# Kernel tuning notes

Hardware: AMD Instinct MI355X
Metric: run time of the kernel (lower is better)

## Reference

```python
import jax, jax.numpy as jnp
import numpy as np

D = 512
N_TISSUES = 200
N_MECH = 6
WINDOW = 32
LN_EPS = 1e-5


def _make_params(key):
    ks = jax.random.split(key, 16)
    p = {}
    def lin(k, fin, fout):
        return jax.random.normal(k, (fin, fout), jnp.float32) * 0.02, jnp.zeros((fout,), jnp.float32)
    for s in ('local', 'regional', 'macro'):
        p[f'ln_g_{s}'] = jnp.ones((D,), jnp.float32)
        p[f'ln_b_{s}'] = jnp.zeros((D,), jnp.float32)
    p['W_fuse'], p['b_fuse'] = lin(ks[0], 3 * D, D)
    p['W_i1'], p['b_i1'] = lin(ks[1], D, D // 2)
    p['W_i2'], p['b_i2'] = lin(ks[2], D // 2, 1)
    p['W_t1'], p['b_t1'] = lin(ks[3], D, D)
    p['W_t2'], p['b_t2'] = lin(ks[4], D, N_TISSUES)
    p['W_m1'], p['b_m1'] = lin(ks[5], D, D // 2)
    p['W_m2'], p['b_m2'] = lin(ks[6], D // 2, N_MECH)
    return p


def setup_inputs() -> dict:
    key = jax.random.key(0)
    ks = jax.random.split(key, 8)
    B, L = 16, 4096
    inp = {}
    names = ['ref_local', 'ref_regional', 'ref_macro', 'alt_local', 'alt_regional', 'alt_macro']
    for i, n in enumerate(names):
        inp[n] = jax.random.normal(ks[i], (B, L, D), jnp.float32)
    inp['variant_pos'] = jax.random.randint(ks[6], (B,), 0, L, jnp.int32)
    inp.update(_make_params(ks[7]))
    return inp


def _diff_pool(ref, alt, pos, gamma, beta):
    # Vectorized version of the per-batch boundary-clamped window gather:
    # window [pos-w, pos+w] intersected with [0, L), diff = alt-ref, mean-pool.
    B, L, Dm = ref.shape
    offs = jnp.arange(-WINDOW, WINDOW + 1)          # (2w+1,)
    idx = pos[:, None] + offs[None, :]               # (B, 2w+1)
    valid = (idx >= 0) & (idx < L)                   # boundary clamp mask
    idxc = jnp.clip(idx, 0, L - 1)
    r = jnp.take_along_axis(ref, idxc[:, :, None], axis=1)   # (B, 2w+1, D)
    a = jnp.take_along_axis(alt, idxc[:, :, None], axis=1)
    diff = (a - r) * valid[:, :, None].astype(ref.dtype)
    pooled = diff.sum(axis=1) / valid.sum(axis=1)[:, None].astype(ref.dtype)  # (B, D)
    mu = pooled.mean(axis=-1, keepdims=True)
    var = ((pooled - mu) ** 2).mean(axis=-1, keepdims=True)
    return (pooled - mu) / jnp.sqrt(var + LN_EPS) * gamma + beta


def _gelu(x):
    return jax.nn.gelu(x, approximate=False)


def reference(ref_local, ref_regional, ref_macro, alt_local, alt_regional, alt_macro,
              variant_pos,
              ln_g_local, ln_b_local, ln_g_regional, ln_b_regional, ln_g_macro, ln_b_macro,
              W_fuse, b_fuse, W_i1, b_i1, W_i2, b_i2,
              W_t1, b_t1, W_t2, b_t2, W_m1, b_m1, W_m2, b_m2):
    d_local = _diff_pool(ref_local, alt_local, variant_pos, ln_g_local, ln_b_local)
    d_reg = _diff_pool(ref_regional, alt_regional, variant_pos, ln_g_regional, ln_b_regional)
    d_mac = _diff_pool(ref_macro, alt_macro, variant_pos, ln_g_macro, ln_b_macro)
    cat = jnp.concatenate([d_local, d_reg, d_mac], axis=-1)   # (B, 3D)
    fused = _gelu(cat @ W_fuse + b_fuse)                       # (B, D); dropout = eval identity
    impact = jax.nn.sigmoid(_gelu(fused @ W_i1 + b_i1) @ W_i2 + b_i2)[:, 0]  # (B,)
    tissue = _gelu(fused @ W_t1 + b_t1) @ W_t2 + b_t2          # (B, n_tissues)
    mech = _gelu(fused @ W_m1 + b_m1) @ W_m2 + b_m2            # (B, 6)
    return impact, tissue, mech, fused
```

## Files before the change

### kernel.cpp

```cpp
#include <hip/hip_runtime.h>
#include <math.h>

#define D 512
#define LSEQ 4096
#define NB 16
#define WINDOW 32
#define NCHUNK 5
#define CHUNK 13
#define N_TISSUES 200
#define N_MECH 6
#define LN_EPS 1e-5f

__device__ __forceinline__ float gelu_exact(float x) {
    return 0.5f * x * (1.0f + erff(x * 0.70710678118654752f));
}

__global__ __launch_bounds__(256) void pool_partial_kernel(
    const float* __restrict__ ref0, const float* __restrict__ ref1, const float* __restrict__ ref2,
    const float* __restrict__ alt0, const float* __restrict__ alt1, const float* __restrict__ alt2,
    const int* __restrict__ pos, float* __restrict__ partial)
{
    const int blk = blockIdx.x;
    const int b = blk / (3 * NCHUNK);
    const int s = (blk / NCHUNK) % 3;
    const int c = blk % NCHUNK;
    const float* __restrict__ ref = (s == 0) ? ref0 : ((s == 1) ? ref1 : ref2);
    const float* __restrict__ alt = (s == 0) ? alt0 : ((s == 1) ? alt1 : alt2);
    const int p = pos[b];
    const int tid = threadIdx.x;

    float acc0 = 0.0f, acc1 = 0.0f;
    const int base_off = -WINDOW + c * CHUNK;
    #pragma unroll
    for (int i = 0; i < CHUNK; ++i) {
        const int idx = p + base_off + i;
        if (idx >= 0 && idx < LSEQ) {
            const size_t row = ((size_t)b * LSEQ + (size_t)idx) * D;
            acc0 += alt[row + tid]       - ref[row + tid];
            acc1 += alt[row + tid + 256] - ref[row + tid + 256];
        }
    }
    float* __restrict__ outp = partial + ((size_t)(b * 3 + s) * NCHUNK + c) * D;
    outp[tid]       = acc0;
    outp[tid + 256] = acc1;
}

__global__ __launch_bounds__(512) void head_kernel(
    const float* __restrict__ partial, const int* __restrict__ pos,
    const float* __restrict__ g0, const float* __restrict__ be0,
    const float* __restrict__ g1, const float* __restrict__ be1,
    const float* __restrict__ g2, const float* __restrict__ be2,
    const float* __restrict__ Wf,  const float* __restrict__ bf,
    const float* __restrict__ Wi1, const float* __restrict__ bi1,
    const float* __restrict__ Wi2, const float* __restrict__ bi2,
    const float* __restrict__ Wt1, const float* __restrict__ bt1,
    const float* __restrict__ Wt2, const float* __restrict__ bt2,
    const float* __restrict__ Wm1, const float* __restrict__ bm1,
    const float* __restrict__ Wm2, const float* __restrict__ bm2,
    float* __restrict__ out)
{
    __shared__ float cat_lds[3 * D];
    __shared__ float fused_lds[D];
    __shared__ float t1_lds[D];
    __shared__ float i1_lds[D / 2];
    __shared__ float m1_lds[D / 2];
    __shared__ float red[16];

    const int b = blockIdx.x;
    const int tid = threadIdx.x;
    const int lane = tid & 63;
    const int wave = tid >> 6;

    const int p = pos[b];
    const int lo = (p - WINDOW < 0) ? 0 : (p - WINDOW);
    const int hi = (p + WINDOW > LSEQ - 1) ? (LSEQ - 1) : (p + WINDOW);
    const float inv_cnt = 1.0f / (float)(hi - lo + 1);

    for (int s = 0; s < 3; ++s) {
        const float* __restrict__ part = partial + (size_t)(b * 3 + s) * NCHUNK * D;
        float v = part[tid] + part[D + tid] + part[2 * D + tid]
                + part[3 * D + tid] + part[4 * D + tid];
        v *= inv_cnt;

        float s1 = v, s2 = v * v;
        #pragma unroll
        for (int o = 32; o > 0; o >>= 1) {
            s1 += __shfl_down(s1, o, 64);
            s2 += __shfl_down(s2, o, 64);
        }
        if (lane == 0) { red[wave] = s1; red[8 + wave] = s2; }
        __syncthreads();
        float t1_ = 0.0f, t2_ = 0.0f;
        #pragma unroll
        for (int w = 0; w < 8; ++w) { t1_ += red[w]; t2_ += red[8 + w]; }
        const float mu = t1_ * (1.0f / (float)D);
        const float var = t2_ * (1.0f / (float)D) - mu * mu;
        const float rstd = rsqrtf(var + LN_EPS);

        const float* __restrict__ g  = (s == 0) ? g0  : ((s == 1) ? g1  : g2);
        const float* __restrict__ be = (s == 0) ? be0 : ((s == 1) ? be1 : be2);
        cat_lds[s * D + tid] = (v - mu) * rstd * g[tid] + be[tid];
        __syncthreads();
    }

    {
        const float4* __restrict__ x4 = (const float4*)cat_lds;
        float a0 = 0.0f, a1 = 0.0f, a2 = 0.0f, a3 = 0.0f;
        #pragma unroll 4
        for (int k4 = 0; k4 < (3 * D) / 4; ++k4) {
            const float4 x = x4[k4];
            const float* __restrict__ w = Wf + (size_t)(4 * k4) * D + tid;
            a0 += x.x * w[0];
            a1 += x.y * w[D];
            a2 += x.z * w[2 * D];
            a3 += x.w * w[3 * D];
        }
        const float acc = bf[tid] + ((a0 + a1) + (a2 + a3));
        const float ge = gelu_exact(acc);
        fused_lds[tid] = ge;
        out[3312 + b * D + tid] = ge;
    }
    __syncthreads();

    {
        const float4* __restrict__ x4 = (const float4*)fused_lds;
        float a0 = 0.0f, a1 = 0.0f, a2 = 0.0f, a3 = 0.0f;
        #pragma unroll 4
        for (int k4 = 0; k4 < D / 4; ++k4) {
            const float4 x = x4[k4];
            const float* __restrict__ w = Wt1 + (size_t)(4 * k4) * D + tid;
            a0 += x.x * w[0];
            a1 += x.y * w[D];
            a2 += x.z * w[2 * D];
            a3 += x.w * w[3 * D];
        }
        t1_lds[tid] = gelu_exact(bt1[tid] + ((a0 + a1) + (a2 + a3)));
    }
    if (tid < 256) {
        const float4* __restrict__ x4 = (const float4*)fused_lds;
        float a0 = 0.0f, a1 = 0.0f, a2 = 0.0f, a3 = 0.0f;
        #pragma unroll 4
        for (int k4 = 0; k4 < D / 4; ++k4) {
            const float4 x = x4[k4];
            const float* __restrict__ w = Wi1 + (size_t)(4 * k4) * 256 + tid;
            a0 += x.x * w[0];
            a1 += x.y * w[256];
            a2 += x.z * w[512];
            a3 += x.w * w[768];
        }
        i1_lds[tid] = gelu_exact(bi1[tid] + ((a0 + a1) + (a2 + a3)));
    } else {
        const int j = tid - 256;
        const float4* __restrict__ x4 = (const float4*)fused_lds;
        float a0 = 0.0f, a1 = 0.0f, a2 = 0.0f, a3 = 0.0f;
        #pragma unroll 4
        for (int k4 = 0; k4 < D / 4; ++k4) {
            const float4 x = x4[k4];
            const float* __restrict__ w = Wm1 + (size_t)(4 * k4) * 256 + j;
            a0 += x.x * w[0];
            a1 += x.y * w[256];
            a2 += x.z * w[512];
            a3 += x.w * w[768];
        }
        m1_lds[j] = gelu_exact(bm1[j] + ((a0 + a1) + (a2 + a3)));
    }
    __syncthreads();

    if (tid < N_TISSUES) {
        const float4* __restrict__ x4 = (const float4*)t1_lds;
        float a0 = 0.0f, a1 = 0.0f, a2 = 0.0f, a3 = 0.0f;
        #pragma unroll 4
        for (int k4 = 0; k4 < D / 4; ++k4) {
            const float4 x = x4[k4];
            const float* __restrict__ w = Wt2 + (size_t)(4 * k4) * N_TISSUES + tid;
            a0 += x.x * w[0];
            a1 += x.y * w[N_TISSUES];
            a2 += x.z * w[2 * N_TISSUES];
            a3 += x.w * w[3 * N_TISSUES];
        }
        out[16 + b * N_TISSUES + tid] = bt2[tid] + ((a0 + a1) + (a2 + a3));
    } else if (tid >= 208 && tid < 208 + N_MECH) {
        const int m = tid - 208;
        const float4* __restrict__ x4 = (const float4*)m1_lds;
        float a0 = 0.0f, a1 = 0.0f, a2 = 0.0f, a3 = 0.0f;
        #pragma unroll 4
        for (int k4 = 0; k4 < 256 / 4; ++k4) {
            const float4 x = x4[k4];
            const float* __restrict__ w = Wm2 + (size_t)(4 * k4) * N_MECH + m;
            a0 += x.x * w[0];
            a1 += x.y * w[N_MECH];
            a2 += x.z * w[2 * N_MECH];
            a3 += x.w * w[3 * N_MECH];
        }
        out[3216 + b * N_MECH + m] = bm2[m] + ((a0 + a1) + (a2 + a3));
    }
    if (tid >= 256) {
        const int t = tid - 256;
        float ip = i1_lds[t] * Wi2[t];
        #pragma unroll
        for (int o = 32; o > 0; o >>= 1) ip += __shfl_down(ip, o, 64);
        if (lane == 0) red[wave] = ip;
    }
    __syncthreads();
    if (tid == 0) {
        const float x = red[4] + red[5] + red[6] + red[7] + bi2[0];
        out[b] = 1.0f / (1.0f + expf(-x));
    }
}

extern "C" void kernel_launch(void* const* d_in, const int* in_sizes, int n_in,
                              void* d_out, int out_size, void* d_ws, size_t ws_size,
                              hipStream_t stream) {
    const float* ref_local    = (const float*)d_in[0];
    const float* ref_regional = (const float*)d_in[1];
    const float* ref_macro    = (const float*)d_in[2];
    const float* alt_local    = (const float*)d_in[3];
    const float* alt_regional = (const float*)d_in[4];
    const float* alt_macro    = (const float*)d_in[5];
    const int*   pos          = (const int*)d_in[6];
    const float* g0  = (const float*)d_in[7];
    const float* be0 = (const float*)d_in[8];
    const float* g1  = (const float*)d_in[9];
    const float* be1 = (const float*)d_in[10];
    const float* g2  = (const float*)d_in[11];
    const float* be2 = (const float*)d_in[12];
    const float* Wf  = (const float*)d_in[13];
    const float* bf  = (const float*)d_in[14];
    const float* Wi1 = (const float*)d_in[15];
    const float* bi1 = (const float*)d_in[16];
    const float* Wi2 = (const float*)d_in[17];
    const float* bi2 = (const float*)d_in[18];
    const float* Wt1 = (const float*)d_in[19];
    const float* bt1 = (const float*)d_in[20];
    const float* Wt2 = (const float*)d_in[21];
    const float* bt2 = (const float*)d_in[22];
    const float* Wm1 = (const float*)d_in[23];
    const float* bm1 = (const float*)d_in[24];
    const float* Wm2 = (const float*)d_in[25];
    const float* bm2 = (const float*)d_in[26];

    float* partial = (float*)d_ws;
    float* out = (float*)d_out;

    pool_partial_kernel<<<NB * 3 * NCHUNK, 256, 0, stream>>>(
        ref_local, ref_regional, ref_macro,
        alt_local, alt_regional, alt_macro, pos, partial);

    head_kernel<<<NB, 512, 0, stream>>>(
        partial, pos, g0, be0, g1, be1, g2, be2,
        Wf, bf, Wi1, bi1, Wi2, bi2, Wt1, bt1, Wt2, bt2, Wm1, bm1, Wm2, bm2,
        out);
}
```

Baseline: 622.5 us.

## Split head MLP into batched split-K GEMM kernels with atomic accumulation

```diff
diff --git a/kernel.cpp b/kernel.cpp
--- a/kernel.cpp
+++ b/kernel.cpp
@@ -11,8 +11,18 @@
 #define N_MECH 6
 #define LN_EPS 1e-5f
 
+#define WS_PARTIAL 0
+#define WS_CAT     122880
+#define WS_FUSED   147456
+#define WS_H1      155648
+#define WS_T2      172032
+#define ZERO_SPAN  27776
+
 __device__ __forceinline__ float gelu_exact(float x) {
     return 0.5f * x * (1.0f + erff(x * 0.70710678118654752f));
+}
+__device__ __forceinline__ void atom_add(float* p, float v) {
+    unsafeAtomicAdd(p, v);
 }
 
 __global__ __launch_bounds__(256) void pool_partial_kernel(
@@ -45,166 +55,208 @@
     outp[tid + 256] = acc1;
 }
 
-__global__ __launch_bounds__(512) void head_kernel(
+__global__ __launch_bounds__(512) void prep_kernel(
     const float* __restrict__ partial, const int* __restrict__ pos,
     const float* __restrict__ g0, const float* __restrict__ be0,
     const float* __restrict__ g1, const float* __restrict__ be1,
     const float* __restrict__ g2, const float* __restrict__ be2,
-    const float* __restrict__ Wf,  const float* __restrict__ bf,
-    const float* __restrict__ Wi1, const float* __restrict__ bi1,
-    const float* __restrict__ Wi2, const float* __restrict__ bi2,
-    const float* __restrict__ Wt1, const float* __restrict__ bt1,
-    const float* __restrict__ Wt2, const float* __restrict__ bt2,
-    const float* __restrict__ Wm1, const float* __restrict__ bm1,
-    const float* __restrict__ Wm2, const float* __restrict__ bm2,
-    float* __restrict__ out)
-{
-    __shared__ float cat_lds[3 * D];
-    __shared__ float fused_lds[D];
-    __shared__ float t1_lds[D];
-    __shared__ float i1_lds[D / 2];
-    __shared__ float m1_lds[D / 2];
+    float* __restrict__ cat, float* __restrict__ zero_base)
+{
     __shared__ float red[16];
-
-    const int b = blockIdx.x;
+    const int blk = blockIdx.x;
+    const int b = blk / 3;
+    const int s = blk % 3;
     const int tid = threadIdx.x;
     const int lane = tid & 63;
     const int wave = tid >> 6;
+
+    for (int i = blk * 512 + tid; i < ZERO_SPAN; i += 48 * 512)
+        zero_base[i] = 0.0f;
 
     const int p = pos[b];
     const int lo = (p - WINDOW < 0) ? 0 : (p - WINDOW);
     const int hi = (p + WINDOW > LSEQ - 1) ? (LSEQ - 1) : (p + WINDOW);
     const float inv_cnt = 1.0f / (float)(hi - lo + 1);
 
-    for (int s = 0; s < 3; ++s) {
-        const float* __restrict__ part = partial + (size_t)(b * 3 + s) * NCHUNK * D;
-        float v = part[tid] + part[D + tid] + part[2 * D + tid]
-                + part[3 * D + tid] + part[4 * D + tid];
-        v *= inv_cnt;
-
-        float s1 = v, s2 = v * v;
+    const float* __restrict__ part = partial + (size_t)(b * 3 + s) * NCHUNK * D;
+    float v = part[tid] + part[D + tid] + part[2 * D + tid]
+            + part[3 * D + tid] + part[4 * D + tid];
+    v *= inv_cnt;
+
+    float s1 = v, s2 = v * v;
+    #pragma unroll
+    for (int o = 32; o > 0; o >>= 1) {
+        s1 += __shfl_down(s1, o, 64);
+        s2 += __shfl_down(s2, o, 64);
+    }
+    if (lane == 0) { red[wave] = s1; red[8 + wave] = s2; }
+    __syncthreads();
+    float t1_ = 0.0f, t2_ = 0.0f;
+    #pragma unroll
+    for (int w = 0; w < 8; ++w) { t1_ += red[w]; t2_ += red[8 + w]; }
+    const float mu = t1_ * (1.0f / (float)D);
+    const float var = t2_ * (1.0f / (float)D) - mu * mu;
+    const float rstd = rsqrtf(var + LN_EPS);
+
+    const float* __restrict__ g  = (s == 0) ? g0  : ((s == 1) ? g1  : g2);
+    const float* __restrict__ be = (s == 0) ? be0 : ((s == 1) ? be1 : be2);
+    cat[(size_t)b * 1536 + s * D + tid] = (v - mu) * rstd * g[tid] + be[tid];
+}
+
+__global__ __launch_bounds__(256) void fused_mm_kernel(
+    const float* __restrict__ cat, const float* __restrict__ Wf,
+    float* __restrict__ fused_raw)
+{
+    __shared__ float xl[16 * 64];
+    const int kc = blockIdx.x >> 1;
+    const int cg = blockIdx.x & 1;
+    const int tid = threadIdx.x;
+
+    {
+        const int e = tid * 4;
+        const int b = e >> 6, kk = e & 63;
+        *(float4*)&xl[e] = *(const float4*)&cat[(size_t)b * 1536 + kc * 64 + kk];
+    }
+    __syncthreads();
+
+    const int col = cg * 256 + tid;
+    float acc[16];
+    #pragma unroll
+    for (int b = 0; b < 16; ++b) acc[b] = 0.0f;
+
+    const float* __restrict__ wp = Wf + (size_t)(kc * 64) * D + col;
+    #pragma unroll 4
+    for (int kk = 0; kk < 64; ++kk) {
+        const float w = wp[(size_t)kk * D];
         #pragma unroll
-        for (int o = 32; o > 0; o >>= 1) {
-            s1 += __shfl_down(s1, o, 64);
-            s2 += __shfl_down(s2, o, 64);
-        }
-        if (lane == 0) { red[wave] = s1; red[8 + wave] = s2; }
+        for (int b = 0; b < 16; ++b) acc[b] += xl[b * 64 + kk] * w;
+    }
+    #pragma unroll
+    for (int b = 0; b < 16; ++b) atom_add(&fused_raw[b * D + col], acc[b]);
+}
+
+__global__ __launch_bounds__(256) void h1_mm_kernel(
+    const float* __restrict__ fused_raw, const float* __restrict__ bf,
+    const float* __restrict__ Wt1, const float* __restrict__ Wi1,
+    const float* __restrict__ Wm1,
+    float* __restrict__ h1_raw, float* __restrict__ out)
+{
+    __shared__ float xl[16 * 64];
+    const int kc = blockIdx.x >> 2;
+    const int cg = blockIdx.x & 3;
+    const int tid = threadIdx.x;
+
+    {
+        const int e = tid * 4;
+        const int b = e >> 6, kk = e & 63;
+        const float4 r = *(const float4*)&fused_raw[(size_t)b * D + kc * 64 + kk];
+        const float4 bb = *(const float4*)&bf[kc * 64 + kk];
+        float4 gg;
+        gg.x = gelu_exact(r.x + bb.x); gg.y = gelu_exact(r.y + bb.y);
+        gg.z = gelu_exact(r.z + bb.z); gg.w = gelu_exact(r.w + bb.w);
+        *(float4*)&xl[e] = gg;
+        if (cg == 0) *(float4*)&out[3312 + (size_t)b * D + kc * 64 + kk] = gg;
+    }
+    __syncthreads();
+
+    const int col = cg * 256 + tid;
+    const float* __restrict__ wp;
+    int ldw;
+    if (cg < 2)      { wp = Wt1 + (size_t)(kc * 64) * D + col;          ldw = D;   }
+    else if (cg == 2){ wp = Wi1 + (size_t)(kc * 64) * 256 + (col - 512); ldw = 256; }
+    else             { wp = Wm1 + (size_t)(kc * 64) * 256 + (col - 768); ldw = 256; }
+
+    float acc[16];
+    #pragma unroll
+    for (int b = 0; b < 16; ++b) acc[b] = 0.0f;
+    #pragma unroll 4
+    for (int kk = 0; kk < 64; ++kk) {
+        const float w = wp[(size_t)kk * ldw];
+        #pragma unroll
+        for (int b = 0; b < 16; ++b) acc[b] += xl[b * 64 + kk] * w;
+    }
+    #pragma unroll
+    for (int b = 0; b < 16; ++b) atom_add(&h1_raw[b * 1024 + col], acc[b]);
+}
+
+__global__ __launch_bounds__(256) void small_heads_kernel(
+    const float* __restrict__ h1_raw,
+    const float* __restrict__ bt1, const float* __restrict__ bi1,
+    const float* __restrict__ bm1,
+    const float* __restrict__ Wt2, const float* __restrict__ Wm2,
+    const float* __restrict__ Wi2, const float* __restrict__ bm2,
+    const float* __restrict__ bi2,
+    float* __restrict__ t2_raw, float* __restrict__ out)
+{
+    __shared__ float s[8192];
+    const int tid = threadIdx.x;
+
+    if (blockIdx.x < 8) {
+        const int kc = blockIdx.x;
+        {
+            const int e = tid * 4;
+            const int b = e >> 6, kk = e & 63;
+            const float4 r = *(const float4*)&h1_raw[(size_t)b * 1024 + kc * 64 + kk];
+            const float4 bb = *(const float4*)&bt1[kc * 64 + kk];
+            s[e]     = gelu_exact(r.x + bb.x);
+            s[e + 1] = gelu_exact(r.y + bb.y);
+            s[e + 2] = gelu_exact(r.z + bb.z);
+            s[e + 3] = gelu_exact(r.w + bb.w);
+        }
         __syncthreads();
-        float t1_ = 0.0f, t2_ = 0.0f;
-        #pragma unroll
-        for (int w = 0; w < 8; ++w) { t1_ += red[w]; t2_ += red[8 + w]; }
-        const float mu = t1_ * (1.0f / (float)D);
-        const float var = t2_ * (1.0f / (float)D) - mu * mu;
-        const float rstd = rsqrtf(var + LN_EPS);
-
-        const float* __restrict__ g  = (s == 0) ? g0  : ((s == 1) ? g1  : g2);
-        const float* __restrict__ be = (s == 0) ? be0 : ((s == 1) ? be1 : be2);
-        cat_lds[s * D + tid] = (v - mu) * rstd * g[tid] + be[tid];
+        if (tid < N_TISSUES) {
+            const float* __restrict__ wp = Wt2 + (size_t)(kc * 64) * N_TISSUES + tid;
+            float acc[16];
+            #pragma unroll
+            for (int b = 0; b < 16; ++b) acc[b] = 0.0f;
+            #pragma unroll 4
+            for (int kk = 0; kk < 64; ++kk) {
+                const float w = wp[(size_t)kk * N_TISSUES];
+                #pragma unroll
+                for (int b = 0; b < 16; ++b) acc[b] += s[b * 64 + kk] * w;
+            }
+            #pragma unroll
+            for (int b = 0; b < 16; ++b) atom_add(&t2_raw[b * N_TISSUES + tid], acc[b]);
+        }
+    } else {
+        for (int b = 0; b < 16; ++b) {
+            s[b * 256 + tid]        = gelu_exact(bi1[tid] + h1_raw[(size_t)b * 1024 + 512 + tid]);
+            s[4096 + b * 256 + tid] = gelu_exact(bm1[tid] + h1_raw[(size_t)b * 1024 + 768 + tid]);
+        }
         __syncthreads();
-    }
-
-    {
-        const float4* __restrict__ x4 = (const float4*)cat_lds;
-        float a0 = 0.0f, a1 = 0.0f, a2 = 0.0f, a3 = 0.0f;
-        #pragma unroll 4
-        for (int k4 = 0; k4 < (3 * D) / 4; ++k4) {
-            const float4 x = x4[k4];
-            const float* __restrict__ w = Wf + (size_t)(4 * k4) * D + tid;
-            a0 += x.x * w[0];
-            a1 += x.y * w[D];
-            a2 += x.z * w[2 * D];
-            a3 += x.w * w[3 * D];
-        }
-        const float acc = bf[tid] + ((a0 + a1) + (a2 + a3));
-        const float ge = gelu_exact(acc);
-        fused_lds[tid] = ge;
-        out[3312 + b * D + tid] = ge;
-    }
-    __syncthreads();
-
-    {
-        const float4* __restrict__ x4 = (const float4*)fused_lds;
-        float a0 = 0.0f, a1 = 0.0f, a2 = 0.0f, a3 = 0.0f;
-        #pragma unroll 4
-        for (int k4 = 0; k4 < D / 4; ++k4) {
-            const float4 x = x4[k4];
-            const float* __restrict__ w = Wt1 + (size_t)(4 * k4) * D + tid;
-            a0 += x.x * w[0];
-            a1 += x.y * w[D];
-            a2 += x.z * w[2 * D];
-            a3 += x.w * w[3 * D];
-        }
-        t1_lds[tid] = gelu_exact(bt1[tid] + ((a0 + a1) + (a2 + a3)));
-    }
-    if (tid < 256) {
-        const float4* __restrict__ x4 = (const float4*)fused_lds;
-        float a0 = 0.0f, a1 = 0.0f, a2 = 0.0f, a3 = 0.0f;
-        #pragma unroll 4
-        for (int k4 = 0; k4 < D / 4; ++k4) {
-            const float4 x = x4[k4];
-            const float* __restrict__ w = Wi1 + (size_t)(4 * k4) * 256 + tid;
-            a0 += x.x * w[0];
-            a1 += x.y * w[256];
-            a2 += x.z * w[512];
-            a3 += x.w * w[768];
-        }
-        i1_lds[tid] = gelu_exact(bi1[tid] + ((a0 + a1) + (a2 + a3)));
-    } else {
-        const int j = tid - 256;
-        const float4* __restrict__ x4 = (const float4*)fused_lds;
-        float a0 = 0.0f, a1 = 0.0f, a2 = 0.0f, a3 = 0.0f;
-        #pragma unroll 4
-        for (int k4 = 0; k4 < D / 4; ++k4) {
-            const float4 x = x4[k4];
-            const float* __restrict__ w = Wm1 + (size_t)(4 * k4) * 256 + j;
-            a0 += x.x * w[0];
-            a1 += x.y * w[256];
-            a2 += x.z * w[512];
-            a3 += x.w * w[768];
-        }
-        m1_lds[j] = gelu_exact(bm1[j] + ((a0 + a1) + (a2 + a3)));
-    }
-    __syncthreads();
-
-    if (tid < N_TISSUES) {
-        const float4* __restrict__ x4 = (const float4*)t1_lds;
-        float a0 = 0.0f, a1 = 0.0f, a2 = 0.0f, a3 = 0.0f;
-        #pragma unroll 4
-        for (int k4 = 0; k4 < D / 4; ++k4) {
-            const float4 x = x4[k4];
-            const float* __restrict__ w = Wt2 + (size_t)(4 * k4) * N_TISSUES + tid;
-            a0 += x.x * w[0];
-            a1 += x.y * w[N_TISSUES];
-            a2 += x.z * w[2 * N_TISSUES];
-            a3 += x.w * w[3 * N_TISSUES];
-        }
-        out[16 + b * N_TISSUES + tid] = bt2[tid] + ((a0 + a1) + (a2 + a3));
-    } else if (tid >= 208 && tid < 208 + N_MECH) {
-        const int m = tid - 208;
-        const float4* __restrict__ x4 = (const float4*)m1_lds;
-        float a0 = 0.0f, a1 = 0.0f, a2 = 0.0f, a3 = 0.0f;
-        #pragma unroll 4
-        for (int k4 = 0; k4 < 256 / 4; ++k4) {
-            const float4 x = x4[k4];
-            const float* __restrict__ w = Wm2 + (size_t)(4 * k4) * N_MECH + m;
-            a0 += x.x * w[0];
-            a1 += x.y * w[N_MECH];
-            a2 += x.z * w[2 * N_MECH];
-            a3 += x.w * w[3 * N_MECH];
-        }
-        out[3216 + b * N_MECH + m] = bm2[m] + ((a0 + a1) + (a2 + a3));
-    }
-    if (tid >= 256) {
-        const int t = tid - 256;
-        float ip = i1_lds[t] * Wi2[t];
-        #pragma unroll
-        for (int o = 32; o > 0; o >>= 1) ip += __shfl_down(ip, o, 64);
-        if (lane == 0) red[wave] = ip;
-    }
-    __syncthreads();
-    if (tid == 0) {
-        const float x = red[4] + red[5] + red[6] + red[7] + bi2[0];
-        out[b] = 1.0f / (1.0f + expf(-x));
+        if (tid < 96) {
+            const int b = tid / 6, m = tid % 6;
+            float a0 = 0, a1 = 0, a2 = 0, a3 = 0;
+            for (int j = 0; j < 256; j += 4) {
+                a0 += s[4096 + b * 256 + j]     * Wm2[(j)     * N_MECH + m];
+                a1 += s[4096 + b * 256 + j + 1] * Wm2[(j + 1) * N_MECH + m];
+                a2 += s[4096 + b * 256 + j + 2] * Wm2[(j + 2) * N_MECH + m];
+                a3 += s[4096 + b * 256 + j + 3] * Wm2[(j + 3) * N_MECH + m];
+            }
+            out[3216 + tid] = bm2[m] + ((a0 + a1) + (a2 + a3));
+        } else if (tid < 112) {
+            const int b = tid - 96;
+            float a0 = 0, a1 = 0, a2 = 0, a3 = 0;
+            for (int j = 0; j < 256; j += 4) {
+                a0 += s[b * 256 + j]     * Wi2[j];
+                a1 += s[b * 256 + j + 1] * Wi2[j + 1];
+                a2 += s[b * 256 + j + 2] * Wi2[j + 2];
+                a3 += s[b * 256 + j + 3] * Wi2[j + 3];
+            }
+            const float x = bi2[0] + ((a0 + a1) + (a2 + a3));
+            out[b] = 1.0f / (1.0f + expf(-x));
+        }
+    }
+}
+
+__global__ __launch_bounds__(256) void t2_final_kernel(
+    const float* __restrict__ t2_raw, const float* __restrict__ bt2,
+    float* __restrict__ out)
+{
+    const int gid = blockIdx.x * 256 + threadIdx.x;
+    if (gid < NB * N_TISSUES) {
+        const int c = gid % N_TISSUES;
+        out[16 + gid] = bt2[c] + t2_raw[gid];
     }
 }
 
@@ -239,15 +291,27 @@
     const float* Wm2 = (const float*)d_in[25];
     const float* bm2 = (const float*)d_in[26];
 
-    float* partial = (float*)d_ws;
-    float* out = (float*)d_out;
+    float* ws        = (float*)d_ws;
+    float* partial   = ws + WS_PARTIAL;
+    float* cat       = ws + WS_CAT;
+    float* fused_raw = ws + WS_FUSED;
+    float* h1_raw    = ws + WS_H1;
+    float* t2_raw    = ws + WS_T2;
+    float* out       = (float*)d_out;
 
     pool_partial_kernel<<<NB * 3 * NCHUNK, 256, 0, stream>>>(
         ref_local, ref_regional, ref_macro,
         alt_local, alt_regional, alt_macro, pos, partial);
 
-    head_kernel<<<NB, 512, 0, stream>>>(
-        partial, pos, g0, be0, g1, be1, g2, be2,
-        Wf, bf, Wi1, bi1, Wi2, bi2, Wt1, bt1, Wt2, bt2, Wm1, bm1, Wm2, bm2,
-        out);
-}
+    prep_kernel<<<48, 512, 0, stream>>>(
+        partial, pos, g0, be0, g1, be1, g2, be2, cat, fused_raw );
+
+    fused_mm_kernel<<<48, 256, 0, stream>>>(cat, Wf, fused_raw);
+
+    h1_mm_kernel<<<32, 256, 0, stream>>>(fused_raw, bf, Wt1, Wi1, Wm1, h1_raw, out);
+
+    small_heads_kernel<<<9, 256, 0, stream>>>(
+        h1_raw, bt1, bi1, bm1, Wt2, Wm2, Wi2, bm2, bi2, t2_raw, out);
+
+    t2_final_kernel<<<13, 256, 0, stream>>>(t2_raw, bt2, out);
+}
```

After: 553.5 us. 1.12x faster.
